# Kernel tuning notes

Measured on AMD Instinct MI355X. Metric: run time of the kernel, lower is better.

The kernel has to match this reference:

```python
import jax, jax.numpy as jnp
import numpy as np

NH = 8
NUM_BLOCKS = 7
EPS = 1e-5


def layer_norm(x, s, b):
    mu = x.mean(-1, keepdims=True)
    var = x.var(-1, keepdims=True)
    return (x - mu) / jnp.sqrt(var + EPS) * s + b


def head_norm(x, scale, nh):
    # GroupNorm over heads (scale only), as used after sLSTM/mLSTM cells
    B, T, D = x.shape
    xh = x.reshape(B, T, nh, D // nh)
    mu = xh.mean(-1, keepdims=True)
    var = xh.var(-1, keepdims=True)
    return ((xh - mu) / jnp.sqrt(var + EPS)).reshape(B, T, D) * scale


def causal_conv(x, w, b):
    # depthwise causal conv1d, kernel K=4; x: (B,T,C), w: (K,C), b: (C,)
    K = w.shape[0]
    T = x.shape[1]
    xp = jnp.pad(x, ((0, 0), (K - 1, 0), (0, 0)))
    out = b
    for k in range(K):
        out = out + xp[:, k:k + T] * w[k]
    return out


def slstm_layer(x, conv_w, conv_b, Wg, Rg, bg, gn_scale):
    # sLSTM: sequential recurrence with exponential gating + stabilizer
    B, T, D = x.shape
    dh = D // NH
    xc = jax.nn.silu(causal_conv(x, conv_w, conv_b))
    i_in = xc @ Wg[0] + bg[0]   # i,f gates see conv features
    f_in = xc @ Wg[1] + bg[1]
    z_in = x @ Wg[2] + bg[2]    # z,o gates see raw input
    o_in = x @ Wg[3] + bg[3]

    def step(carry, xs):
        h, c, n, m = carry
        ix, fx, zx, ox = xs
        hh = h.reshape(B, NH, dh)
        rec = jnp.einsum('bhd,ghde->gbhe', hh, Rg).reshape(4, B, D)
        it = ix + rec[0]
        ft = fx + rec[1]
        zt = jnp.tanh(zx + rec[2])
        ot = jax.nn.sigmoid(ox + rec[3])
        m_new = jnp.maximum(ft + m, it)
        ig = jnp.exp(it - m_new)
        fg = jnp.exp(ft + m - m_new)
        c_new = fg * c + ig * zt
        n_new = fg * n + ig
        h_new = ot * c_new / jnp.maximum(n_new, 1e-6)
        return (h_new, c_new, n_new, m_new), h_new

    init = tuple(jnp.zeros((B, D), x.dtype) for _ in range(4))
    xs = tuple(jnp.swapaxes(a, 0, 1) for a in (i_in, f_in, z_in, o_in))
    _, hs = jax.lax.scan(step, init, xs)
    return head_norm(jnp.swapaxes(hs, 0, 1), gn_scale, NH)


def mlstm_layer(x, w_up, conv_w, conv_b, wq, wk, wv, w_if, b_if, skip, gn_scale, w_down):
    # mLSTM: matrix-memory cell in parallel stabilized (attention-like) form
    B, T, D = x.shape
    xm, z = jnp.split(x @ w_up, 2, axis=-1)
    DI = xm.shape[-1]
    dh = DI // NH
    xc = jax.nn.silu(causal_conv(xm, conv_w, conv_b))
    hw = lambda inp, w: jnp.einsum('bthd,hde->bthe', inp.reshape(B, T, NH, dh), w)
    q = hw(xc, wq)
    k = hw(xc, wk) / jnp.sqrt(jnp.asarray(dh, x.dtype))
    v = hw(xm, wv)
    gates = xc @ w_if + b_if                          # (B,T,2*NH)
    logi = jnp.swapaxes(gates[..., :NH], 1, 2)        # (B,NH,T)
    logf = jax.nn.log_sigmoid(jnp.swapaxes(gates[..., NH:], 1, 2))
    cf = jnp.cumsum(logf, axis=-1)                    # (B,NH,T)
    Dm = cf[:, :, :, None] - cf[:, :, None, :] + logi[:, :, None, :]
    tri = jnp.tril(jnp.ones((T, T), bool))
    Dm = jnp.where(tri, Dm, -jnp.inf)
    m = Dm.max(-1)                                    # (B,NH,T) row stabilizer
    S = jnp.einsum('bthd,bshd->bhts', q, k) * jnp.exp(Dm - m[..., None])
    norm = jnp.maximum(jnp.abs(S.sum(-1)), jnp.exp(-m))
    h = jnp.einsum('bhts,bshd->bthd', S / norm[..., None], v).reshape(B, T, DI)
    h = head_norm(h, gn_scale, NH) + skip * xc        # learnable skip of conv branch
    return (h * jax.nn.silu(z)) @ w_down              # output gate + down-proj


def _forward(x, w_in, b_in, ln_in_s, ln_in_b, s_ln_s, s_ln_b, s_conv_w, s_conv_b,
             s_wg, s_rg, s_bg, s_gn, s_ffln_s, s_ffln_b, s_ff_w1, s_ff_w2,
             m_ln_s, m_ln_b, m_w_up, m_conv_w, m_conv_b, m_wq, m_wk, m_wv,
             m_w_if, m_b_if, m_skip, m_gn, m_w_down, post_ln_s, post_ln_b,
             hw1, hb1, hw2, hb2, hw3, hb3):
    h = layer_norm(x @ w_in + b_in, ln_in_s, ln_in_b)
    si = mi = 0
    for blk in range(NUM_BLOCKS):
        if blk % 2 == 0:
            y = slstm_layer(layer_norm(h, s_ln_s[si], s_ln_b[si]),
                            s_conv_w[si], s_conv_b[si], s_wg[si], s_rg[si], s_bg[si], s_gn[si])
            h = h + y
            u = layer_norm(h, s_ffln_s[si], s_ffln_b[si]) @ s_ff_w1[si]
            g, up = jnp.split(u, 2, axis=-1)
            h = h + (jax.nn.gelu(g) * up) @ s_ff_w2[si]   # gated FFN (proj 4/3)
            si += 1
        else:
            h = h + mlstm_layer(layer_norm(h, m_ln_s[mi], m_ln_b[mi]),
                                m_w_up[mi], m_conv_w[mi], m_conv_b[mi], m_wq[mi], m_wk[mi],
                                m_wv[mi], m_w_if[mi], m_b_if[mi], m_skip[mi], m_gn[mi],
                                m_w_down[mi])
            mi += 1
    h = layer_norm(h, post_ln_s, post_ln_b)
    last = h[:, -1, :]

    def head(w1, b1, w2, b2, w3, b3):
        a = jax.nn.gelu(last @ w1 + b1)
        a = jax.nn.gelu(a @ w2 + b2)
        return a @ w3 + b3

    preds = jax.vmap(head)(hw1, hb1, hw2, hb2, hw3, hb3)  # (H,B,1)
    return jnp.squeeze(preds, -1).T                       # (B,H) horizons stacked


def setup_inputs() -> dict:
    key = jax.random.key(0)
    ks = iter(jax.random.split(key, 64))

    def nrm(shape, scale):
        return jax.random.normal(next(ks), shape, jnp.float32) * scale

    B, T, F, D = 32, 252, 8, 512
    DH = D // NH
    DI = 2 * D
    DHI = DI // NH
    FF = int(D * 4 / 3)
    H = 6
    nS, nM = 4, 3
    p = {}
    p['x'] = nrm((B, T, F), 1.0)
    p['w_in'] = nrm((F, D), 0.3)
    p['b_in'] = jnp.zeros((D,))
    p['ln_in_s'] = jnp.ones((D,))
    p['ln_in_b'] = jnp.zeros((D,))
    p['s_ln_s'] = jnp.ones((nS, D))
    p['s_ln_b'] = jnp.zeros((nS, D))
    p['s_conv_w'] = nrm((nS, 4, D), 0.3)
    p['s_conv_b'] = jnp.zeros((nS, D))
    p['s_wg'] = nrm((nS, 4, D, D), 0.04)
    p['s_rg'] = nrm((nS, 4, NH, DH, DH), 0.1)
    p['s_bg'] = nrm((nS, 4, D), 0.1)
    p['s_gn'] = jnp.ones((nS, D))
    p['s_ffln_s'] = jnp.ones((nS, D))
    p['s_ffln_b'] = jnp.zeros((nS, D))
    p['s_ff_w1'] = nrm((nS, D, 2 * FF), 0.04)
    p['s_ff_w2'] = nrm((nS, FF, D), 0.04)
    p['m_ln_s'] = jnp.ones((nM, D))
    p['m_ln_b'] = jnp.zeros((nM, D))
    p['m_w_up'] = nrm((nM, D, 2 * DI), 0.04)
    p['m_conv_w'] = nrm((nM, 4, DI), 0.3)
    p['m_conv_b'] = jnp.zeros((nM, DI))
    p['m_wq'] = nrm((nM, NH, DHI, DHI), 0.09)
    p['m_wk'] = nrm((nM, NH, DHI, DHI), 0.09)
    p['m_wv'] = nrm((nM, NH, DHI, DHI), 0.09)
    p['m_w_if'] = nrm((nM, DI, 2 * NH), 0.03)
    p['m_b_if'] = jnp.zeros((nM, 2 * NH))
    p['m_skip'] = jnp.ones((nM, DI))
    p['m_gn'] = jnp.ones((nM, DI))
    p['m_w_down'] = nrm((nM, DI, D), 0.03)
    p['post_ln_s'] = jnp.ones((D,))
    p['post_ln_b'] = jnp.zeros((D,))
    p['hw1'] = nrm((H, D, D // 2), 0.04)
    p['hb1'] = jnp.zeros((H, D // 2))
    p['hw2'] = nrm((H, D // 2, D // 4), 0.06)
    p['hb2'] = jnp.zeros((H, D // 4))
    p['hw3'] = nrm((H, D // 4, 1), 0.09)
    p['hb3'] = jnp.zeros((H, 1))
    return p


def reference(x, w_in, b_in, ln_in_s, ln_in_b, s_ln_s, s_ln_b, s_conv_w, s_conv_b,
              s_wg, s_rg, s_bg, s_gn, s_ffln_s, s_ffln_b, s_ff_w1, s_ff_w2,
              m_ln_s, m_ln_b, m_w_up, m_conv_w, m_conv_b, m_wq, m_wk, m_wv,
              m_w_if, m_b_if, m_skip, m_gn, m_w_down, post_ln_s, post_ln_b,
              hw1, hb1, hw2, hb2, hw3, hb3):
    return _forward(x, w_in, b_in, ln_in_s, ln_in_b, s_ln_s, s_ln_b, s_conv_w, s_conv_b,
                    s_wg, s_rg, s_bg, s_gn, s_ffln_s, s_ffln_b, s_ff_w1, s_ff_w2,
                    m_ln_s, m_ln_b, m_w_up, m_conv_w, m_conv_b, m_wq, m_wk, m_wv,
                    m_w_if, m_b_if, m_skip, m_gn, m_w_down, post_ln_s, post_ln_b,
                    hw1, hb1, hw2, hb2, hw3, hb3)
```

## Files before the change

### kernel.cpp

```cpp
#include <hip/hip_runtime.h>
#include <hip/hip_bf16.h>
#include <cmath>

typedef __hip_bfloat16 bf16;

#define B_   32
#define T_   252
#define F_   8
#define D_   512
#define NH_  8
#define DH_  64
#define DI_  1024
#define DHI_ 128
#define FF_  682
#define FF2_ 1364
#define FFP_ 704
#define BT_  (B_*T_)
#define EPS_ 1e-5f

typedef __attribute__((ext_vector_type(8))) short short8;
typedef __attribute__((ext_vector_type(4))) float floatx4;

__device__ __forceinline__ float b2f(bf16 v){ return __bfloat162float(v); }
__device__ __forceinline__ float siluf(float x){ return x/(1.f+expf(-x)); }
__device__ __forceinline__ float geluf(float x){
  float x3 = x*x*x;
  return 0.5f*x*(1.f+tanhf(0.7978845608028654f*(x+0.044715f*x3)));
}
__device__ __forceinline__ float ldin(const void* p, long i, int isbf){
  return isbf ? __bfloat162float(((const bf16*)p)[i]) : ((const float*)p)[i];
}
__device__ __forceinline__ unsigned short f2bu(float f){
  bf16 h = __float2bfloat16(f);
  return *(reinterpret_cast<unsigned short*>(&h));
}
__device__ __forceinline__ void split2(float v, unsigned short& h, unsigned short& l){
  bf16 hb = __float2bfloat16(v);
  h = *(reinterpret_cast<unsigned short*>(&hb));
  float r = v - __bfloat162float(hb);
  bf16 lb = __float2bfloat16(r);
  l = *(reinterpret_cast<unsigned short*>(&lb));
}
__device__ __forceinline__ unsigned packbf(float x, float y){
  return (unsigned)f2bu(x) | ((unsigned)f2bu(y) << 16);
}

__global__ void detect_dtype(const unsigned* __restrict__ probe, int* __restrict__ flag)
{
  if (threadIdx.x == 0) *flag = (*probe == 0x3F803F80u) ? 1 : 0;
}

__global__ __launch_bounds__(256) void wt_transpose2(
    const void* __restrict__ in, long inOff, long inStride, int K, int N, int outK,
    unsigned short* __restrict__ outHi, unsigned short* __restrict__ outLo,
    long outStride, const int* __restrict__ dflag)
{
  const int isbf = *dflag;
  const int bz = blockIdx.z;
  const long base = inOff + (long)bz*inStride;
  unsigned short* oh = outHi + (long)bz*outStride;
  unsigned short* ol = outLo ? outLo + (long)bz*outStride : nullptr;
  __shared__ float tile[32][33];
  const int k0 = blockIdx.y*32, n0 = blockIdx.x*32;
  const int tn = threadIdx.x & 31, tk = threadIdx.x >> 5;
#pragma unroll
  for (int i=0;i<4;i++){
    int kk = tk + i*8;
    float v = 0.f;
    if (k0+kk < K && n0+tn < N) v = ldin(in, base + (long)(k0+kk)*N + n0+tn, isbf);
    tile[kk][tn] = v;
  }
  __syncthreads();
#pragma unroll
  for (int i=0;i<4;i++){
    int nn = tk + i*8;
    if (n0+nn < N && k0+tn < outK){
      unsigned short h, l;
      split2(tile[tn][nn], h, l);
      oh[(long)(n0+nn)*outK + k0+tn] = h;
      if (ol) ol[(long)(n0+nn)*outK + k0+tn] = l;
    }
  }
}

__global__ __launch_bounds__(256) void gemm_split(
    const float* __restrict__ A0, const float* __restrict__ A1, int zSplit, long strideA,
    const unsigned short* __restrict__ Bhi, const unsigned short* __restrict__ Blo,
    const void* __restrict__ bias, long offBias, float* __restrict__ C,
    int N, int K, int lda, int ldc,
    long strideBT, long strideC, long strideBias,
    float alpha, int flags, int splitB, const int* __restrict__ dflag)
{
  const int isbf = *dflag;
  const int bz = blockIdx.z;
  const float* A = ((bz < zSplit) ? A0 : A1) + (long)bz*strideA;
  const unsigned short* bhp = Bhi + (long)bz*strideBT;
  const unsigned short* blp = Blo + (long)bz*strideBT;
  const long cBase = (long)bz*strideC;
  const long bBias = offBias + (long)bz*strideBias;

  __shared__ unsigned short aH[64*72], aL[64*72], bH[64*72], bL[64*72];
  const int tid = threadIdx.x;
  const int wid = tid >> 6, lane = tid & 63;
  const int wm = (wid >> 1)*32, wn = (wid & 1)*32;
  const int m0 = blockIdx.y*64, n0 = blockIdx.x*64;
  const int lr = lane & 15, lq = lane >> 4;

  floatx4 acc[2][2];
#pragma unroll
  for (int mi=0;mi<2;mi++)
#pragma unroll
    for (int ni=0;ni<2;ni++)
#pragma unroll
      for (int r=0;r<4;r++) acc[mi][ni][r] = 0.f;

  const int sRow = tid >> 2;
  const int sSeg = (tid & 3)*16;

  for (int k0 = 0; k0 < K; k0 += 64) {
    {
      const float* ap = A + (long)(m0 + sRow)*lda + k0 + sSeg;
#pragma unroll
      for (int c=0;c<4;c++){
        const float4 v = *(const float4*)(ap + c*4);
        unsigned short h0,h1,h2,h3,l0,l1,l2,l3;
        split2(v.x,h0,l0); split2(v.y,h1,l1); split2(v.z,h2,l2); split2(v.w,h3,l3);
        uint2 ph, pl;
        ph.x = (unsigned)h0 | ((unsigned)h1<<16); ph.y = (unsigned)h2 | ((unsigned)h3<<16);
        pl.x = (unsigned)l0 | ((unsigned)l1<<16); pl.y = (unsigned)l2 | ((unsigned)l3<<16);
        *(uint2*)&aH[sRow*72 + sSeg + c*4] = ph;
        *(uint2*)&aL[sRow*72 + sSeg + c*4] = pl;
      }
    }
    {
      const int gn = n0 + sRow;
      const bool nv = gn < N;
      const long bo = (long)gn*K + k0 + sSeg;
      uint4 z4; z4.x=z4.y=z4.z=z4.w=0;
      uint4 h0 = nv ? *(const uint4*)(bhp + bo)     : z4;
      uint4 h1 = nv ? *(const uint4*)(bhp + bo + 8) : z4;
      *(uint4*)&bH[sRow*72 + sSeg]     = h0;
      *(uint4*)&bH[sRow*72 + sSeg + 8] = h1;
      if (splitB){
        uint4 l0_ = nv ? *(const uint4*)(blp + bo)     : z4;
        uint4 l1_ = nv ? *(const uint4*)(blp + bo + 8) : z4;
        *(uint4*)&bL[sRow*72 + sSeg]     = l0_;
        *(uint4*)&bL[sRow*72 + sSeg + 8] = l1_;
      }
    }
    __syncthreads();

#pragma unroll
    for (int ks=0;ks<2;ks++){
      short8 ah[2], al[2], bh_[2], bl_[2];
#pragma unroll
      for (int mi=0;mi<2;mi++){
        ah[mi] = *(const short8*)&aH[(wm+mi*16+lr)*72 + ks*32 + lq*8];
        al[mi] = *(const short8*)&aL[(wm+mi*16+lr)*72 + ks*32 + lq*8];
      }
#pragma unroll
      for (int ni=0;ni<2;ni++){
        bh_[ni] = *(const short8*)&bH[(wn+ni*16+lr)*72 + ks*32 + lq*8];
        if (splitB) bl_[ni] = *(const short8*)&bL[(wn+ni*16+lr)*72 + ks*32 + lq*8];
      }
#pragma unroll
      for (int mi=0;mi<2;mi++)
#pragma unroll
        for (int ni=0;ni<2;ni++){
          acc[mi][ni] = __builtin_amdgcn_mfma_f32_16x16x32_bf16(al[mi], bh_[ni], acc[mi][ni], 0,0,0);
          if (splitB)
            acc[mi][ni] = __builtin_amdgcn_mfma_f32_16x16x32_bf16(ah[mi], bl_[ni], acc[mi][ni], 0,0,0);
          acc[mi][ni] = __builtin_amdgcn_mfma_f32_16x16x32_bf16(ah[mi], bh_[ni], acc[mi][ni], 0,0,0);
        }
    }
    __syncthreads();
  }

#pragma unroll
  for (int mi=0;mi<2;mi++){
#pragma unroll
    for (int ni=0;ni<2;ni++){
      const int gn = n0 + wn + ni*16 + lr;
      if (gn >= N) continue;
      const float bv = (flags & 1) ? ldin(bias, bBias + gn, isbf) : 0.f;
#pragma unroll
      for (int rr=0;rr<4;rr++){
        const int gm = m0 + wm + mi*16 + lq*4 + rr;
        float vv = acc[mi][ni][rr]*alpha + bv;
        const long idx = cBase + (long)gm*ldc + gn;
        if (flags & 8) {
          ((unsigned short*)C)[idx] = f2bu(vv);
        } else {
          if (flags & 2) vv += C[idx];
          C[idx] = vv;
        }
      }
    }
  }
}

__global__ __launch_bounds__(256) void ln_proj(
    const void* __restrict__ x, const void* __restrict__ w,
    const void* __restrict__ bb, const void* __restrict__ s,
    const void* __restrict__ b, float* __restrict__ out,
    const int* __restrict__ dflag)
{
  const int isbf = *dflag;
  const int r = blockIdx.x;
  const int tid = threadIdx.x;
  float xr[8];
#pragma unroll
  for (int f = 0; f < 8; f++) xr[f] = ldin(x, (long)r*8+f, isbf);
  float vv[2];
#pragma unroll
  for (int i2 = 0; i2 < 2; i2++) {
    const int j = tid + i2*256;
    float a = ldin(bb, j, isbf);
#pragma unroll
    for (int f = 0; f < 8; f++) a += xr[f]*ldin(w, f*512+j, isbf);
    vv[i2] = a;
  }
  __shared__ float r1[256], r2[256];
  r1[tid] = vv[0]+vv[1]; r2[tid] = vv[0]*vv[0]+vv[1]*vv[1];
  __syncthreads();
  for (int o = 128; o > 0; o >>= 1) {
    if (tid < o) { r1[tid]+=r1[tid+o]; r2[tid]+=r2[tid+o]; }
    __syncthreads();
  }
  const float mu = r1[0]*(1.f/512.f);
  const float var = r2[0]*(1.f/512.f)-mu*mu;
  const float rstd = rsqrtf(var+EPS_);
  float* orow = out + (long)r*512;
#pragma unroll
  for (int i2 = 0; i2 < 2; i2++) {
    const int j = tid + i2*256;
    orow[j] = (vv[i2]-mu)*rstd*ldin(s, j, isbf) + ldin(b, j, isbf);
  }
}

__global__ __launch_bounds__(256) void ln_rows(
    const float* __restrict__ in, long rowStride,
    const void* __restrict__ s, long offS,
    const void* __restrict__ b, long offB,
    float* __restrict__ out, const int* __restrict__ dflag)
{
  const int isbf = *dflag;
  const long r = blockIdx.x;
  const int tid = threadIdx.x;
  const float* xr = in + r*rowStride;
  const float v0 = xr[tid], v1 = xr[tid+256];
  __shared__ float r1[256], r2[256];
  r1[tid] = v0+v1; r2[tid] = v0*v0+v1*v1;
  __syncthreads();
  for (int o = 128; o > 0; o >>= 1) {
    if (tid < o) { r1[tid]+=r1[tid+o]; r2[tid]+=r2[tid+o]; }
    __syncthreads();
  }
  const float mu = r1[0]*(1.f/512.f);
  const float var = r2[0]*(1.f/512.f)-mu*mu;
  const float rstd = rsqrtf(var+EPS_);
  float* orow = out + r*(long)D_;
  orow[tid]     = (v0-mu)*rstd*ldin(s, offS+tid, isbf)     + ldin(b, offB+tid, isbf);
  orow[tid+256] = (v1-mu)*rstd*ldin(s, offS+tid+256, isbf) + ldin(b, offB+tid+256, isbf);
}

__global__ void conv_silu(const float* __restrict__ in, int inStride,
                          const void* __restrict__ w, long offW,
                          const void* __restrict__ bias, long offBias,
                          float* __restrict__ out, int Dc,
                          const int* __restrict__ dflag)
{
  const int isbf = *dflag;
  const long total = (long)BT_ * Dc;
  for (long idx = (long)blockIdx.x*256 + threadIdx.x; idx < total;
       idx += (long)gridDim.x*256) {
    const int d = (int)(idx % Dc);
    const long bt = idx / Dc;
    const int b = (int)(bt / T_), t = (int)(bt % T_);
    float a = ldin(bias, offBias + d, isbf);
#pragma unroll
    for (int kk = 0; kk < 4; kk++) {
      const int ts = t - 3 + kk;
      if (ts >= 0) a += ldin(w, offW + kk*Dc + d, isbf) * in[((long)(b*T_+ts))*inStride + d];
    }
    out[idx] = siluf(a);
  }
}

__global__ __launch_bounds__(256) void gemm_f32b(
    const float* __restrict__ A, const void* __restrict__ Bw, long offB,
    const void* __restrict__ bias, long offBias, float* __restrict__ C,
    int M, int N, int K, int lda, int ldb, int ldc,
    long strideA, long strideB, long strideC, long strideBias,
    float alpha, int flags, const int* __restrict__ dflag)
{
  const int isbf = *dflag;
  const int bz = blockIdx.z;
  A  += (long)bz * strideA;
  const long bB = offB + (long)bz * strideB;
  const long cBase = (long)bz * strideC;
  const long bBias = offBias + (long)bz * strideBias;
  __shared__ float sA[16][68];
  __shared__ float sB[16][64];
  const int tid = threadIdx.x;
  const int tx = tid & 15, ty = tid >> 4;
  const int m0 = blockIdx.y * 64, n0 = blockIdx.x * 64;
  float acc[4][4];
#pragma unroll
  for (int i=0;i<4;i++)
#pragma unroll
    for (int j=0;j<4;j++) acc[i][j]=0.f;

  for (int k0 = 0; k0 < K; k0 += 16) {
#pragma unroll
    for (int r = 0; r < 4; r++) {
      int lin = tid + r*256;
      int kk = lin & 15, m = lin >> 4;
      int gm = m0 + m, gk = k0 + kk;
      sA[kk][m] = (gm < M && gk < K) ? A[(long)gm*lda + gk] : 0.f;
    }
#pragma unroll
    for (int r = 0; r < 4; r++) {
      int lin = tid + r*256;
      int nn = lin & 63, kk = lin >> 6;
      int gn = n0 + nn, gk = k0 + kk;
      sB[kk][nn] = (gn < N && gk < K) ? ldin(Bw, bB + (long)gk*ldb + gn, isbf) : 0.f;
    }
    __syncthreads();
#pragma unroll
    for (int kk = 0; kk < 16; kk++) {
      const float4 a4 = *(const float4*)(&sA[kk][ty*4]);
      const float4 b4 = *(const float4*)(&sB[kk][tx*4]);
      float av[4] = {a4.x, a4.y, a4.z, a4.w};
      float bv[4] = {b4.x, b4.y, b4.z, b4.w};
#pragma unroll
      for (int i=0;i<4;i++)
#pragma unroll
        for (int j=0;j<4;j++) acc[i][j] += av[i]*bv[j];
    }
    __syncthreads();
  }
#pragma unroll
  for (int i=0;i<4;i++) {
    const int gm = m0 + ty*4 + i;
    if (gm >= M) continue;
#pragma unroll
    for (int j=0;j<4;j++) {
      const int gn = n0 + tx*4 + j;
      if (gn >= N) continue;
      float vv = acc[i][j]*alpha;
      if (flags & 1) vv += ldin(bias, bBias + gn, isbf);
      if (flags & 4) vv = geluf(vv);
      const long idx = cBase + (long)gm*ldc + gn;
      if (flags & 8) {
        ((unsigned short*)C)[idx] = f2bu(vv);
      } else {
        if (flags & 2) vv += C[idx];
        C[idx] = vv;
      }
    }
  }
}

__global__ __launch_bounds__(256) void slstm_scan(
    const float* __restrict__ g4, const void* __restrict__ Rg, long offR,
    float* __restrict__ hs, const int* __restrict__ dflag)
{
  const int isbf = *dflag;
  const int blk = blockIdx.x;
  const int b = blk >> 3, hd = blk & 7;
  const int tid = threadIdx.x;
  const int g = tid >> 6, e = tid & 63;
  float w[64];
  {
    const long wp = offR + ((long)(g*NH_ + hd)*64)*64 + e;
#pragma unroll
    for (int d = 0; d < 64; d++) w[d] = ldin(Rg, wp + d*64, isbf);
  }
  __shared__ float hlds[64];
  __shared__ float rec[4][64];
  if (tid < 64) hlds[tid] = 0.f;
  float c = 0.f, n = 0.f, m = 0.f;
  __syncthreads();
  const long gate_base = (long)(b*T_)*D_ + hd*64 + e;
  for (int t = 0; t < T_; t++) {
    float r = 0.f;
#pragma unroll
    for (int d4 = 0; d4 < 16; d4++) {
      const float4 hv = *(const float4*)(&hlds[d4*4]);
      r += w[4*d4]*hv.x + w[4*d4+1]*hv.y + w[4*d4+2]*hv.z + w[4*d4+3]*hv.w;
    }
    r += g4[(long)g*BT_*D_ + gate_base + (long)t*D_];
    rec[g][e] = r;
    __syncthreads();
    if (tid < 64) {
      const float it = rec[0][e], ft = rec[1][e];
      const float zt = tanhf(rec[2][e]);
      const float ot = 1.f/(1.f+expf(-rec[3][e]));
      const float mn = fmaxf(ft + m, it);
      const float ig = expf(it - mn);
      const float fg = expf(ft + m - mn);
      c = fg*c + ig*zt;
      n = fg*n + ig;
      m = mn;
      const float hn = ot*c/fmaxf(n, 1e-6f);
      hlds[e] = hn;
      hs[(long)(b*T_+t)*D_ + hd*64 + e] = hn;
    }
    __syncthreads();
  }
}

__global__ __launch_bounds__(64) void hn_add(
    const float* __restrict__ hs, const void* __restrict__ gn, long offG,
    float* __restrict__ h, const int* __restrict__ dflag)
{
  const int isbf = *dflag;
  const int blk = blockIdx.x;
  const int bt = blk >> 3, hd = blk & 7;
  const int e = threadIdx.x;
  const long idx = (long)bt*D_ + hd*64 + e;
  const float x = hs[idx];
  float s1 = x, s2 = x*x;
#pragma unroll
  for (int o = 32; o > 0; o >>= 1) { s1 += __shfl_xor(s1, o); s2 += __shfl_xor(s2, o); }
  const float mu = s1*(1.f/64.f);
  const float var = s2*(1.f/64.f) - mu*mu;
  const float y = (x-mu)*rsqrtf(var+EPS_)*ldin(gn, offG + hd*64+e, isbf);
  h[idx] += y;
}

__global__ void ffgate(const float* __restrict__ u, float* __restrict__ out)
{
  const long total = (long)BT_*FFP_;
  for (long idx = (long)blockIdx.x*256 + threadIdx.x; idx < total;
       idx += (long)gridDim.x*256) {
    const long m = idx / FFP_;
    const int j = (int)(idx % FFP_);
    float r = 0.f;
    if (j < FF_) {
      const float g = u[m*FF2_ + j];
      r = geluf(g) * u[m*FF2_ + FF_ + j];
    }
    out[idx] = r;
  }
}

__global__ __launch_bounds__(256) void mlstm_cf(
    const float* __restrict__ g16, float* __restrict__ cf, float* __restrict__ logi)
{
  const int bh = blockIdx.x;
  const int b = bh >> 3, hd = bh & 7;
  const int tid = threadIdx.x;
  __shared__ float slf[T_];
  if (tid < T_) {
    const float gf = g16[(long)(b*T_+tid)*16 + 8 + hd];
    const float ls = (gf >= 0.f) ? -log1pf(expf(-gf)) : (gf - log1pf(expf(gf)));
    slf[tid] = ls;
    logi[(long)bh*T_ + tid] = g16[(long)(b*T_+tid)*16 + hd];
  }
  __syncthreads();
  if (tid == 0) {
    float a = 0.f;
    for (int t = 0; t < T_; t++) { a += slf[t]; slf[t] = a; }
  }
  __syncthreads();
  if (tid < T_) cf[(long)bh*T_ + tid] = slf[tid];
}

#define QPD 136
#define VPD 72
__global__ __launch_bounds__(256) void attn_mfma(
    const float* __restrict__ q, const unsigned short* __restrict__ k,
    const unsigned short* __restrict__ v, const float* __restrict__ cf,
    const float* __restrict__ li, float* __restrict__ hatt)
{
  const int tt = blockIdx.x, bh = blockIdx.y;
  const int b = bh >> 3, hd = bh & 7;
  const int t0 = tt*64;
  const int tid = threadIdx.x;
  const int w = tid >> 6, lane = tid & 63;
  const int lr = lane & 15, lq = lane >> 4;

  __shared__ unsigned short sQ[64*QPD];
  __shared__ unsigned short sK[64*QPD];
  __shared__ unsigned short sVt[128*VPD];
  __shared__ unsigned short sS[64*VPD];
  __shared__ float scft[64], scfs[64], slis[64];

  for (int idx = tid; idx < 64*64; idx += 256){
    int r = idx >> 6, dp = idx & 63;
    int t = t0 + r;
    unsigned pk = 0;
    if (t < T_){
      const float* qp = q + ((long)(b*T_+t))*DI_ + hd*DHI_ + dp*2;
      pk = packbf(qp[0], qp[1]);
    }
    *(unsigned*)&sQ[r*QPD + dp*2] = pk;
  }
  if (tid < 64) scft[tid] = (t0+tid < T_) ? cf[(long)bh*T_ + t0+tid] : 0.f;

  float m_st[4], s_st[4], alpha_[4];
#pragma unroll
  for (int rr=0;rr<4;rr++){ m_st[rr] = -INFINITY; s_st[rr] = 0.f; }
  floatx4 accO[8];
#pragma unroll
  for (int nd=0;nd<8;nd++)
#pragma unroll
    for (int rr=0;rr<4;rr++) accO[nd][rr] = 0.f;

  for (int st = 0; st <= tt; st++){
    const int s0 = st*64;
    for (int idx = tid; idx < 64*64; idx += 256){
      int r = idx >> 6, dp = idx & 63;
      int s = s0 + r;
      unsigned pkk = 0, pkv = 0;
      if (s < T_){
        const long base = ((long)(b*T_+s))*DI_ + hd*DHI_ + dp*2;
        pkk = *(const unsigned*)&k[base];
        pkv = *(const unsigned*)&v[base];
      }
      *(unsigned*)&sK[r*QPD + dp*2] = pkk;
      sVt[(dp*2)*VPD + r]   = (unsigned short)(pkv & 0xFFFFu);
      sVt[(dp*2+1)*VPD + r] = (unsigned short)(pkv >> 16);
    }
    if (tid < 64){
      int s = s0 + tid;
      scfs[tid] = (s < T_) ? cf[(long)bh*T_ + s] : 0.f;
      slis[tid] = (s < T_) ? li[(long)bh*T_ + s] : 0.f;
    }
    __syncthreads();

    floatx4 accS[4];
#pragma unroll
    for (int ni=0;ni<4;ni++)
#pragma unroll
      for (int rr=0;rr<4;rr++) accS[ni][rr] = 0.f;
    const int qrow = w*16 + lr;
#pragma unroll
    for (int k0=0;k0<4;k0++){
      short8 a = *(const short8*)&sQ[qrow*QPD + k0*32 + lq*8];
#pragma unroll
      for (int ni=0;ni<4;ni++){
        short8 bb = *(const short8*)&sK[(ni*16+lr)*QPD + k0*32 + lq*8];
        accS[ni] = __builtin_amdgcn_mfma_f32_16x16x32_bf16(a, bb, accS[ni], 0,0,0);
      }
    }

#pragma unroll
    for (int rr=0;rr<4;rr++){
      const int tg = t0 + w*16 + lq*4 + rr;
      const float cftr = scft[w*16 + lq*4 + rr];
      float dmv[4];
      float mx = -INFINITY;
#pragma unroll
      for (int ni=0;ni<4;ni++){
        const int sg = s0 + ni*16 + lr;
        const bool valid = (tg < T_) && (sg <= tg);
        dmv[ni] = valid ? (cftr - scfs[ni*16+lr] + slis[ni*16+lr]) : -INFINITY;
        mx = fmaxf(mx, dmv[ni]);
      }
      mx = fmaxf(mx, __shfl_xor(mx, 1));
      mx = fmaxf(mx, __shfl_xor(mx, 2));
      mx = fmaxf(mx, __shfl_xor(mx, 4));
      mx = fmaxf(mx, __shfl_xor(mx, 8));
      const float mnew = fmaxf(m_st[rr], mx);
      const float al = (mnew == -INFINITY) ? 0.f : expf(m_st[rr] - mnew);
      float rs = 0.f;
#pragma unroll
      for (int ni=0;ni<4;ni++){
        const float wexp = (dmv[ni] == -INFINITY) ? 0.f : expf(dmv[ni] - mnew);
        const float pv = accS[ni][rr]*wexp;
        rs += pv;
        sS[(w*16 + lq*4 + rr)*VPD + ni*16 + lr] = f2bu(pv);
      }
      rs += __shfl_xor(rs, 1);
      rs += __shfl_xor(rs, 2);
      rs += __shfl_xor(rs, 4);
      rs += __shfl_xor(rs, 8);
      s_st[rr] = s_st[rr]*al + rs;
      m_st[rr] = mnew;
      alpha_[rr] = al;
    }

#pragma unroll
    for (int nd=0;nd<8;nd++)
#pragma unroll
      for (int rr=0;rr<4;rr++) accO[nd][rr] *= alpha_[rr];

#pragma unroll
    for (int ks=0;ks<2;ks++){
      short8 aP = *(const short8*)&sS[(w*16 + lr)*VPD + ks*32 + lq*8];
#pragma unroll
      for (int nd=0;nd<8;nd++){
        short8 bV = *(const short8*)&sVt[(nd*16+lr)*VPD + ks*32 + lq*8];
        accO[nd] = __builtin_amdgcn_mfma_f32_16x16x32_bf16(aP, bV, accO[nd], 0,0,0);
      }
    }
    __syncthreads();
  }

#pragma unroll
  for (int rr=0;rr<4;rr++){
    const int tg = t0 + w*16 + lq*4 + rr;
    if (tg >= T_) continue;
    const float inv = 1.f / fmaxf(fabsf(s_st[rr]), expf(-m_st[rr]));
    float* op = hatt + ((long)(b*T_+tg))*DI_ + hd*DHI_;
#pragma unroll
    for (int nd=0;nd<8;nd++)
      op[nd*16 + lr] = accO[nd][rr]*inv;
  }
}

__global__ __launch_bounds__(128) void hn_mlstm(
    const float* __restrict__ hatt, const void* __restrict__ gn, long offG,
    const void* __restrict__ skip, long offSk, const float* __restrict__ xc,
    const float* __restrict__ u, float* __restrict__ gin,
    const int* __restrict__ dflag)
{
  const int isbf = *dflag;
  const int blk = blockIdx.x;
  const int bt = blk >> 3, hd = blk & 7;
  const int e = threadIdx.x;
  const int j = hd*DHI_ + e;
  const long idx = (long)bt*DI_ + j;
  const float x = hatt[idx];
  __shared__ float r1[128], r2[128];
  r1[e]=x; r2[e]=x*x; __syncthreads();
  for (int o=64;o>0;o>>=1){ if(e<o){r1[e]+=r1[e+o]; r2[e]+=r2[e+o];} __syncthreads(); }
  const float mu = r1[0]*(1.f/128.f);
  const float var = r2[0]*(1.f/128.f)-mu*mu;
  const float y = (x-mu)*rsqrtf(var+EPS_)*ldin(gn, offG+j, isbf) + ldin(skip, offSk+j, isbf)*xc[idx];
  const float z = u[(long)bt*2048 + DI_ + j];
  gin[idx] = y * siluf(z);
}

__global__ void out_transpose(const float* __restrict__ hp, void* __restrict__ out,
                              const int* __restrict__ dflag)
{
  const int isbf = *dflag;
  const int tid = threadIdx.x;
  if (tid < B_*6) {
    const int b = tid / 6, hd = tid % 6;
    const float v = hp[hd*B_ + b];
    if (isbf) ((bf16*)out)[tid] = __float2bfloat16(v);
    else      ((float*)out)[tid] = v;
  }
}

extern "C" void kernel_launch(void* const* d_in, const int* in_sizes, int n_in,
                              void* d_out, int out_size, void* d_ws, size_t ws_size,
                              hipStream_t stream)
{
  (void)in_sizes; (void)n_in; (void)out_size;
  const void* x        = d_in[0];
  const void* w_in     = d_in[1];
  const void* b_in     = d_in[2];
  const void* ln_in_s  = d_in[3];
  const void* ln_in_b  = d_in[4];
  const void* s_ln_s   = d_in[5];
  const void* s_ln_b   = d_in[6];
  const void* s_conv_w = d_in[7];
  const void* s_conv_b = d_in[8];
  const void* s_wg     = d_in[9];
  const void* s_rg     = d_in[10];
  const void* s_bg     = d_in[11];
  const void* s_gn     = d_in[12];
  const void* s_ffln_s = d_in[13];
  const void* s_ffln_b = d_in[14];
  const void* s_ff_w1  = d_in[15];
  const void* s_ff_w2  = d_in[16];
  const void* m_ln_s   = d_in[17];
  const void* m_ln_b   = d_in[18];
  const void* m_w_up   = d_in[19];
  const void* m_conv_w = d_in[20];
  const void* m_conv_b = d_in[21];
  const void* m_wq     = d_in[22];
  const void* m_wk     = d_in[23];
  const void* m_wv     = d_in[24];
  const void* m_w_if   = d_in[25];
  const void* m_b_if   = d_in[26];
  const void* m_skip   = d_in[27];
  const void* m_gn     = d_in[28];
  const void* m_w_down = d_in[29];
  const void* post_ln_s= d_in[30];
  const void* post_ln_b= d_in[31];
  const void* hw1      = d_in[32];
  const void* hb1      = d_in[33];
  const void* hw2      = d_in[34];
  const void* hb2      = d_in[35];
  const void* hw3      = d_in[36];
  const void* hb3      = d_in[37];

  float* W   = (float*)d_ws;
  float* h   = W;
  float* xn  = W + 4128768L;
  float* xc  = W + 8257536L;
  float* u   = W + 16515072L;
  float* q   = W + 33030144L;
  unsigned short* kk_ = (unsigned short*)(W + 41287680L);
  unsigned short* vv_ = (unsigned short*)(W + 45416448L);
  float* g16 = W + 49545216L;
  float* cfb = W + 49674240L;
  float* lib = W + 49738752L;
  float* last= W + 49803264L;
  float* ha1 = W + 49819648L;
  float* ha2 = W + 49868800L;
  float* hp  = W + 49893376L;
  int*   dfl = (int*)(W + 49893568L);

  const long PLANE = 14327808L;
  unsigned short* wtHi = (unsigned short*)(W + 49893632L);
  unsigned short* wtLo = wtHi + PLANE;
  const long oWg=0, oF1=4194304L, oF2=6987776L, oUp=8429568L;
  const long oQ=11575296L, oK=11968512L, oV=12361728L, oDn=12754944L;

  const size_t needFull = (size_t)49893632L*4 + (size_t)PLANE*4;
  const size_t needMid  = (size_t)49893632L*4 + (size_t)PLANE*2;
  const int tier = (ws_size >= needFull) ? 2 : ((ws_size >= needMid) ? 1 : 0);
  const int spB = (tier == 2) ? 1 : 0;
  unsigned short* loArg = (tier == 2) ? wtLo : nullptr;

  const float kscale = 0.08838834764831845f;

  detect_dtype<<<1, 64, 0, stream>>>((const unsigned*)ln_in_s, dfl);

  if (tier >= 1) {
    wt_transpose2<<<dim3(16,16,16),256,0,stream>>>(s_wg, 0, 262144L, 512, 512, 512,
        wtHi+oWg, loArg?loArg+oWg:nullptr, 262144L, dfl);
    wt_transpose2<<<dim3(43,16,4),256,0,stream>>>(s_ff_w1, 0, 698368L, 512, 1364, 512,
        wtHi+oF1, loArg?loArg+oF1:nullptr, 698368L, dfl);
    wt_transpose2<<<dim3(16,22,4),256,0,stream>>>(s_ff_w2, 0, 349184L, 682, 512, 704,
        wtHi+oF2, loArg?loArg+oF2:nullptr, 360448L, dfl);
    wt_transpose2<<<dim3(64,16,3),256,0,stream>>>(m_w_up, 0, 1048576L, 512, 2048, 512,
        wtHi+oUp, loArg?loArg+oUp:nullptr, 1048576L, dfl);
    wt_transpose2<<<dim3(4,4,24),256,0,stream>>>(m_wq, 0, 16384L, 128, 128, 128,
        wtHi+oQ, loArg?loArg+oQ:nullptr, 16384L, dfl);
    wt_transpose2<<<dim3(4,4,24),256,0,stream>>>(m_wk, 0, 16384L, 128, 128, 128,
        wtHi+oK, loArg?loArg+oK:nullptr, 16384L, dfl);
    wt_transpose2<<<dim3(4,4,24),256,0,stream>>>(m_wv, 0, 16384L, 128, 128, 128,
        wtHi+oV, loArg?loArg+oV:nullptr, 16384L, dfl);
    wt_transpose2<<<dim3(16,32,3),256,0,stream>>>(m_w_down, 0, 524288L, 1024, 512, 1024,
        wtHi+oDn, loArg?loArg+oDn:nullptr, 524288L, dfl);
  }

  ln_proj<<<BT_, 256, 0, stream>>>(x, w_in, b_in, ln_in_s, ln_in_b, h, dfl);

  int si = 0, mi = 0;
  for (int blk = 0; blk < 7; blk++) {
    if ((blk & 1) == 0) {
      ln_rows<<<BT_,256,0,stream>>>(h, 512L, s_ln_s, (long)si*512, s_ln_b, (long)si*512, xn, dfl);
      {
        long tot = (long)BT_*512; int g = (int)((tot+255)/256);
        conv_silu<<<g,256,0,stream>>>(xn, 512, s_conv_w, (long)si*4*512, s_conv_b, (long)si*512, xc, 512, dfl);
      }
      if (tier >= 1) {
        gemm_split<<<dim3(8,126,4),256,0,stream>>>(xc, xn, 2, 0L,
            wtHi+oWg+(long)si*4*262144L, wtLo+oWg+(long)si*4*262144L,
            s_bg, (long)si*4*512, u,
            512, 512, 512, 512, 262144L, (long)BT_*512, 512L, 1.f, 1, spB, dfl);
      } else {
        for (int g = 0; g < 4; g++) {
          const float* Ain = (g < 2) ? xc : xn;
          gemm_f32b<<<dim3(8,126,1),256,0,stream>>>(Ain, s_wg, ((long)(si*4+g))*512*512,
              s_bg, (long)(si*4+g)*512, u + (long)g*BT_*512,
              BT_, 512, 512, 512, 512, 512, 0,0,0,0, 1.f, 1, dfl);
        }
      }
      slstm_scan<<<256,256,0,stream>>>(u, s_rg, (long)si*4*8*64*64, q , dfl);
      hn_add<<<BT_*8,64,0,stream>>>(q, s_gn, (long)si*512, h, dfl);
      ln_rows<<<BT_,256,0,stream>>>(h, 512L, s_ffln_s, (long)si*512, s_ffln_b, (long)si*512, xn, dfl);
      if (tier >= 1)
        gemm_split<<<dim3(22,126,1),256,0,stream>>>(xn, xn, 9, 0L,
            wtHi+oF1+(long)si*698368L, wtLo+oF1+(long)si*698368L, nullptr, 0,
            u, 1364, 512, 512, 1364, 0,0,0, 1.f, 0, spB, dfl);
      else
        gemm_f32b<<<dim3(22,126,1),256,0,stream>>>(xn, s_ff_w1, (long)si*512*1364, nullptr, 0,
            u, BT_, 1364, 512, 512, 1364, 1364, 0,0,0,0, 1.f, 0, dfl);
      {
        long tot = (long)BT_*FFP_; int g = (int)((tot+255)/256);
        ffgate<<<g,256,0,stream>>>(u, q );
      }
      if (tier >= 1)
        gemm_split<<<dim3(8,126,1),256,0,stream>>>(q, q, 9, 0L,
            wtHi+oF2+(long)si*360448L, wtLo+oF2+(long)si*360448L, nullptr, 0,
            h, 512, 704, 704, 512, 0,0,0, 1.f, 2, spB, dfl);
      else
        gemm_f32b<<<dim3(8,126,1),256,0,stream>>>(q, s_ff_w2, (long)si*682*512, nullptr, 0,
            h, BT_, 512, 682, 704, 512, 512, 0,0,0,0, 1.f, 2, dfl);
      si++;
    } else {
      ln_rows<<<BT_,256,0,stream>>>(h, 512L, m_ln_s, (long)mi*512, m_ln_b, (long)mi*512, xn, dfl);
      if (tier >= 1)
        gemm_split<<<dim3(32,126,1),256,0,stream>>>(xn, xn, 9, 0L,
            wtHi+oUp+(long)mi*1048576L, wtLo+oUp+(long)mi*1048576L, nullptr, 0,
            u, 2048, 512, 512, 2048, 0,0,0, 1.f, 0, spB, dfl);
      else
        gemm_f32b<<<dim3(32,126,1),256,0,stream>>>(xn, m_w_up, (long)mi*512*2048, nullptr, 0,
            u, BT_, 2048, 512, 512, 2048, 2048, 0,0,0,0, 1.f, 0, dfl);
      {
        long tot = (long)BT_*1024; int g = (int)((tot+255)/256);
        conv_silu<<<g,256,0,stream>>>(u, 2048, m_conv_w, (long)mi*4*1024, m_conv_b, (long)mi*1024, xc, 1024, dfl);
      }
      if (tier >= 1) {
        gemm_split<<<dim3(2,126,8),256,0,stream>>>(xc, xc, 9, 128L,
            wtHi+oQ+(long)mi*131072L, wtLo+oQ+(long)mi*131072L, nullptr, 0,
            q, 128, 128, 1024, 1024, 16384L, 128L, 0, 1.f, 0, spB, dfl);
        gemm_split<<<dim3(2,126,8),256,0,stream>>>(xc, xc, 9, 128L,
            wtHi+oK+(long)mi*131072L, wtLo+oK+(long)mi*131072L, nullptr, 0,
            (float*)kk_, 128, 128, 1024, 1024, 16384L, 128L, 0, kscale, 8, spB, dfl);
        gemm_split<<<dim3(2,126,8),256,0,stream>>>(u, u, 9, 128L,
            wtHi+oV+(long)mi*131072L, wtLo+oV+(long)mi*131072L, nullptr, 0,
            (float*)vv_, 128, 128, 2048, 1024, 16384L, 128L, 0, 1.f, 8, spB, dfl);
      } else {
        gemm_f32b<<<dim3(2,126,8),256,0,stream>>>(xc, m_wq, (long)mi*8*128*128, nullptr, 0,
            q, BT_, 128, 128, 1024, 128, 1024, 128, 16384, 128, 0, 1.f, 0, dfl);
        gemm_f32b<<<dim3(2,126,8),256,0,stream>>>(xc, m_wk, (long)mi*8*128*128, nullptr, 0,
            (float*)kk_, BT_, 128, 128, 1024, 128, 1024, 128, 16384, 128, 0, kscale, 8, dfl);
        gemm_f32b<<<dim3(2,126,8),256,0,stream>>>(u, m_wv, (long)mi*8*128*128, nullptr, 0,
            (float*)vv_, BT_, 128, 128, 2048, 128, 1024, 128, 16384, 128, 0, 1.f, 8, dfl);
      }
      gemm_f32b<<<dim3(1,126,1),256,0,stream>>>(xc, m_w_if, (long)mi*1024*16, m_b_if, (long)mi*16,
            g16, BT_, 16, 1024, 1024, 16, 16, 0,0,0,0, 1.f, 1, dfl);
      mlstm_cf<<<256,256,0,stream>>>(g16, cfb, lib);
      attn_mfma<<<dim3(4,256),256,0,stream>>>(q, kk_, vv_, cfb, lib, q );
      hn_mlstm<<<BT_*8,128,0,stream>>>(q, m_gn, (long)mi*1024, m_skip, (long)mi*1024, xc, u, q, dfl);
      if (tier >= 1)
        gemm_split<<<dim3(8,126,1),256,0,stream>>>(q, q, 9, 0L,
            wtHi+oDn+(long)mi*524288L, wtLo+oDn+(long)mi*524288L, nullptr, 0,
            h, 512, 1024, 1024, 512, 0,0,0, 1.f, 2, spB, dfl);
      else
        gemm_f32b<<<dim3(8,126,1),256,0,stream>>>(q, m_w_down, (long)mi*1024*512, nullptr, 0,
            h, BT_, 512, 1024, 1024, 512, 512, 0,0,0,0, 1.f, 2, dfl);
      mi++;
    }
  }

  ln_rows<<<B_,256,0,stream>>>(h + (long)(T_-1)*512, (long)T_*512, post_ln_s, 0, post_ln_b, 0, last, dfl);

  gemm_f32b<<<dim3(4,1,6),256,0,stream>>>(last, hw1, 0, hb1, 0, ha1, 32, 256, 512, 512, 256, 256,
        0, 512L*256, 32L*256, 256, 1.f, 1|4, dfl);
  gemm_f32b<<<dim3(2,1,6),256,0,stream>>>(ha1, hw2, 0, hb2, 0, ha2, 32, 128, 256, 256, 128, 128,
        32L*256, 256L*128, 32L*128, 128, 1.f, 1|4, dfl);
  gemm_f32b<<<dim3(1,1,6),256,0,stream>>>(ha2, hw3, 0, hb3, 0, hp, 32, 1, 128, 128, 1, 1,
        32L*128, 128L, 32L, 1, 1.f, 1, dfl);
  out_transpose<<<1,256,0,stream>>>(hp, d_out, dfl);
}
```

Baseline: 4.055 ms.

## Add two-gate-per-thread sLSTM scan using pre-transposed recurrent weights

Adds a prep kernel that transposes each 64x64 recurrent weight block into fp32 workspace so each output column's weights are contiguous. A new scan kernel then uses 128 threads per (batch, head) block, each holding two gates' weight columns in registers. Each thread reads the hidden state from LDS as float4 and prefetches the next step's gate inputs. This halves the thread count per block and vectorises the loads on the serial recurrence path. In exchange it raises register pressure (128 weight floats per thread) and shifts the workspace layout, which changes the tier thresholds.

Measured after the change: 4.261 ms. 1.05x slower.

```diff
diff --git a/kernel.cpp b/kernel.cpp
--- a/kernel.cpp
+++ b/kernel.cpp
@@ -48,6 +48,27 @@
 __global__ void detect_dtype(const unsigned* __restrict__ probe, int* __restrict__ flag)
 {
   if (threadIdx.x == 0) *flag = (*probe == 0x3F803F80u) ? 1 : 0;
+}
+
+__global__ __launch_bounds__(256) void rg_prep(
+    const void* __restrict__ Rg, float* __restrict__ out, const int* __restrict__ dflag)
+{
+  const int isbf = *dflag;
+  const int c = blockIdx.x;
+  const long base = (long)c*4096;
+  __shared__ float tl[64][65];
+  const int col = threadIdx.x & 63, r4 = threadIdx.x >> 6;
+#pragma unroll
+  for (int i=0;i<16;i++){
+    int d = i*4 + r4;
+    tl[d][col] = ldin(Rg, base + (long)d*64 + col, isbf);
+  }
+  __syncthreads();
+#pragma unroll
+  for (int i=0;i<16;i++){
+    int e = i*4 + r4;
+    out[base + (long)e*64 + col] = tl[col][e];
+  }
 }
 
 __global__ __launch_bounds__(256) void wt_transpose2(
@@ -359,6 +380,73 @@
         C[idx] = vv;
       }
     }
+  }
+}
+
+__global__ __launch_bounds__(128, 1) void slstm_scan2(
+    const float* __restrict__ g4, const float* __restrict__ wR,
+    float* __restrict__ hs)
+{
+  const int blk = blockIdx.x;
+  const int b = blk >> 3, hd = blk & 7;
+  const int tid = threadIdx.x;
+  const int e = tid & 63, gp = tid >> 6;
+
+  float w0[64], w1[64];
+  {
+    const float* p0 = wR + (((long)(gp*2)*8 + hd)*64 + e)*64;
+    const float* p1 = wR + (((long)(gp*2+1)*8 + hd)*64 + e)*64;
+#pragma unroll
+    for (int d4 = 0; d4 < 16; d4++){
+      const float4 a = *(const float4*)(p0 + d4*4);
+      const float4 c = *(const float4*)(p1 + d4*4);
+      w0[d4*4+0]=a.x; w0[d4*4+1]=a.y; w0[d4*4+2]=a.z; w0[d4*4+3]=a.w;
+      w1[d4*4+0]=c.x; w1[d4*4+1]=c.y; w1[d4*4+2]=c.z; w1[d4*4+3]=c.w;
+    }
+  }
+
+  __shared__ float hlds[64];
+  __shared__ float rec[4][64];
+  if (tid < 64) hlds[tid] = 0.f;
+  float c = 0.f, n = 0.f, m = 0.f;
+  __syncthreads();
+
+  const long gbase = (long)(b*T_)*D_ + hd*64 + e;
+  const long go0 = (long)(gp*2)*BT_*D_ + gbase;
+  const long go1 = (long)(gp*2+1)*BT_*D_ + gbase;
+  float gn0 = g4[go0], gn1 = g4[go1];
+
+  for (int t = 0; t < T_; t++) {
+    const float gc0 = gn0, gc1 = gn1;
+    if (t+1 < T_) {
+      gn0 = g4[go0 + (long)(t+1)*D_];
+      gn1 = g4[go1 + (long)(t+1)*D_];
+    }
+    float r0 = gc0, r1 = gc1;
+#pragma unroll
+    for (int d4 = 0; d4 < 16; d4++) {
+      const float4 hv = *(const float4*)(&hlds[d4*4]);
+      r0 += w0[4*d4]*hv.x + w0[4*d4+1]*hv.y + w0[4*d4+2]*hv.z + w0[4*d4+3]*hv.w;
+      r1 += w1[4*d4]*hv.x + w1[4*d4+1]*hv.y + w1[4*d4+2]*hv.z + w1[4*d4+3]*hv.w;
+    }
+    rec[gp*2][e] = r0;
+    rec[gp*2+1][e] = r1;
+    __syncthreads();
+    if (tid < 64) {
+      const float it = rec[0][e], ft = rec[1][e];
+      const float zt = tanhf(rec[2][e]);
+      const float ot = 1.f/(1.f+expf(-rec[3][e]));
+      const float mn = fmaxf(ft + m, it);
+      const float ig = expf(it - mn);
+      const float fg = expf(ft + m - mn);
+      c = fg*c + ig*zt;
+      n = fg*n + ig;
+      m = mn;
+      const float hn = ot*c/fmaxf(n, 1e-6f);
+      hlds[e] = hn;
+      hs[(long)(b*T_+t)*D_ + hd*64 + e] = hn;
+    }
+    __syncthreads();
   }
 }
 
@@ -708,15 +796,16 @@
   float* ha2 = W + 49868800L;
   float* hp  = W + 49893376L;
   int*   dfl = (int*)(W + 49893568L);
+  float* wsRg = W + 49893632L;
 
   const long PLANE = 14327808L;
-  unsigned short* wtHi = (unsigned short*)(W + 49893632L);
+  unsigned short* wtHi = (unsigned short*)(W + 50417920L);
   unsigned short* wtLo = wtHi + PLANE;
   const long oWg=0, oF1=4194304L, oF2=6987776L, oUp=8429568L;
   const long oQ=11575296L, oK=11968512L, oV=12361728L, oDn=12754944L;
 
-  const size_t needFull = (size_t)49893632L*4 + (size_t)PLANE*4;
-  const size_t needMid  = (size_t)49893632L*4 + (size_t)PLANE*2;
+  const size_t needFull = (size_t)(50417920L + PLANE)*4;
+  const size_t needMid  = (size_t)(50417920L + PLANE/2)*4 + PLANE;
   const int tier = (ws_size >= needFull) ? 2 : ((ws_size >= needMid) ? 1 : 0);
   const int spB = (tier == 2) ? 1 : 0;
   unsigned short* loArg = (tier == 2) ? wtLo : nullptr;
@@ -726,6 +815,7 @@
   detect_dtype<<<1, 64, 0, stream>>>((const unsigned*)ln_in_s, dfl);
 
   if (tier >= 1) {
+    rg_prep<<<128, 256, 0, stream>>>(s_rg, wsRg, dfl);
     wt_transpose2<<<dim3(16,16,16),256,0,stream>>>(s_wg, 0, 262144L, 512, 512, 512,
         wtHi+oWg, loArg?loArg+oWg:nullptr, 262144L, dfl);
     wt_transpose2<<<dim3(43,16,4),256,0,stream>>>(s_ff_w1, 0, 698368L, 512, 1364, 512,
@@ -767,7 +857,10 @@
               BT_, 512, 512, 512, 512, 512, 0,0,0,0, 1.f, 1, dfl);
         }
       }
-      slstm_scan<<<256,256,0,stream>>>(u, s_rg, (long)si*4*8*64*64, q , dfl);
+      if (tier >= 1)
+        slstm_scan2<<<256,128,0,stream>>>(u, wsRg + (long)si*131072L, q );
+      else
+        slstm_scan<<<256,256,0,stream>>>(u, s_rg, (long)si*4*8*64*64, q , dfl);
       hn_add<<<BT_*8,64,0,stream>>>(q, s_gn, (long)si*512, h, dfl);
       ln_rows<<<BT_,256,0,stream>>>(h, 512L, s_ffln_s, (long)si*512, s_ffln_b, (long)si*512, xn, dfl);
       if (tier >= 1)
```
